# Kernel optimization log

Hardware: AMD Instinct MI355X
Metric: run time of the kernel (lower is better)

## Reference

```python
import jax, jax.numpy as jnp
import numpy as np
from jax import lax

B, S, N, DIM = 4, 512, 16, 8
D_MODEL, D_STATE = 1024, 64
INPUT_SIZE = N * DIM
LN_EPS = 1e-5


def setup_inputs() -> dict:
    key = jax.random.key(0)
    ks = jax.random.split(key, 8)
    s = 0.02
    x = jax.random.normal(ks[0], (B, S, N, DIM), dtype=jnp.float32)
    W_emb = jax.random.normal(ks[1], (INPUT_SIZE, D_MODEL), dtype=jnp.float32) * s
    b_emb = jnp.zeros((D_MODEL,), jnp.float32)
    W_xp = jax.random.normal(ks[2], (D_MODEL, 2 * D_STATE + 1), dtype=jnp.float32) * s
    b_xp = jnp.zeros((2 * D_STATE + 1,), jnp.float32)
    # A init: -exp(arange(1, d_state+1) * 0.1), matching the torch module
    A = -jnp.exp(jnp.arange(1, D_STATE + 1, dtype=jnp.float32) * 0.1)
    Dp = jnp.ones((D_MODEL,), jnp.float32)
    gamma = jnp.ones((D_MODEL,), jnp.float32)
    beta = jnp.zeros((D_MODEL,), jnp.float32)
    W_out = jax.random.normal(ks[3], (D_MODEL, INPUT_SIZE), dtype=jnp.float32) * s
    b_out = jnp.zeros((INPUT_SIZE,), jnp.float32)
    return {"x": x, "W_emb": W_emb, "b_emb": b_emb, "W_xp": W_xp, "b_xp": b_xp,
            "A": A, "Dp": Dp, "gamma": gamma, "beta": beta,
            "W_out": W_out, "b_out": b_out}


def reference(x, W_emb, b_emb, W_xp, b_xp, A, Dp, gamma, beta, W_out, b_out):
    b, s, n, dim = x.shape
    d_state = A.shape[0]
    d_model = W_emb.shape[1]
    u = x.reshape(b, s, n * dim) @ W_emb + b_emb            # [B,S,dm]
    sel = u @ W_xp + b_xp                                    # [B,S,2*ds+1]
    delta = jax.nn.softplus(sel[..., 0:1]) * 0.01            # [B,S,1]
    Bs = sel[..., 1:1 + d_state]                             # [B,S,ds]
    Cs = sel[..., 1 + d_state:]                              # [B,S,ds]
    A_bar = jnp.exp(delta * A)                               # [B,S,ds]
    B_bar = delta * Bs                                       # [B,S,ds]

    def step(h, inp):
        a_t, b_t, c_t, u_t = inp                             # [B,ds],[B,ds],[B,ds],[B,dm]
        h = h * a_t[:, None, :] + b_t[:, None, :] * u_t[:, :, None]  # [B,dm,ds]
        y_t = jnp.einsum('bmd,bd->bm', h, c_t) + u_t * Dp
        return h, y_t

    h0 = jnp.zeros((b, d_model, d_state), x.dtype)
    xs = (jnp.swapaxes(A_bar, 0, 1), jnp.swapaxes(B_bar, 0, 1),
          jnp.swapaxes(Cs, 0, 1), jnp.swapaxes(u, 0, 1))
    _, ys = lax.scan(step, h0, xs)                           # ys: [S,B,dm]
    y = jnp.swapaxes(ys, 0, 1)                               # [B,S,dm]
    mu = y.mean(-1, keepdims=True)
    var = y.var(-1, keepdims=True)
    yn = (y - mu) / jnp.sqrt(var + LN_EPS) * gamma + beta
    pred = yn @ W_out + b_out                                # [B,S,N*D]
    return pred.reshape(b, s, n, dim)
```

## Files before the change

kernel.cpp:

```cpp
#include <hip/hip_runtime.h>
#include <cstddef>

constexpr int ROWS = 2048;
constexpr int NTC  = 16;
constexpr int CL   = 32;

__global__ __launch_bounds__(256)
void k0_rearrange(const float* __restrict__ Wxp,
                  float* __restrict__ wBC, float* __restrict__ wd) {
  int idx = blockIdx.x * 256 + threadIdx.x;
  if (idx >= 1024 * 129) return;
  int k = idx / 129;
  int c = idx - k * 129;
  float v = Wxp[idx];
  if (c == 0) wd[k] = v;
  else        wBC[k * 128 + (c - 1)] = v;
}

template<bool SPLIT>
__global__ __launch_bounds__(256)
void gemm_f32(const float* __restrict__ A, const float* __restrict__ Bm,
              const float* __restrict__ bias, float* __restrict__ C,
              int M, int N, int K, int kchunk) {
  __shared__ float As[32][68];
  __shared__ float Bs[32][68];
  const int t  = threadIdx.x;
  const int n0 = blockIdx.x * 64;
  const int m0 = blockIdx.y * 64;
  int k0 = 0, kend = K;
  if (SPLIT) { k0 = blockIdx.z * kchunk; kend = k0 + kchunk; }
  const int tx = t & 15, ty = t >> 4;
  const int arow = t >> 3, acol = (t & 7) << 2;
  const int brow = t >> 4, bcol = (t & 15) << 2;
  float acc[4][4] = {{0.f}};

  for (int kt = k0; kt < kend; kt += 32) {
    float4 a0 = *(const float4*)&A[(size_t)(m0 + arow)      * K + kt + acol];
    float4 a1 = *(const float4*)&A[(size_t)(m0 + arow + 32) * K + kt + acol];
    float4 b0 = *(const float4*)&Bm[(size_t)(kt + brow)      * N + n0 + bcol];
    float4 b1 = *(const float4*)&Bm[(size_t)(kt + brow + 16) * N + n0 + bcol];
    __syncthreads();
    As[acol + 0][arow] = a0.x; As[acol + 1][arow] = a0.y;
    As[acol + 2][arow] = a0.z; As[acol + 3][arow] = a0.w;
    As[acol + 0][arow + 32] = a1.x; As[acol + 1][arow + 32] = a1.y;
    As[acol + 2][arow + 32] = a1.z; As[acol + 3][arow + 32] = a1.w;
    *(float4*)&Bs[brow][bcol]      = b0;
    *(float4*)&Bs[brow + 16][bcol] = b1;
    __syncthreads();
    #pragma unroll
    for (int k = 0; k < 32; ++k) {
      float4 av = *(const float4*)&As[k][ty << 2];
      float4 bv = *(const float4*)&Bs[k][tx << 2];
      float a_[4] = {av.x, av.y, av.z, av.w};
      float b_[4] = {bv.x, bv.y, bv.z, bv.w};
      #pragma unroll
      for (int i = 0; i < 4; ++i)
        #pragma unroll
        for (int j = 0; j < 4; ++j)
          acc[i][j] = fmaf(a_[i], b_[j], acc[i][j]);
    }
  }

  float* Cp = C;
  if (SPLIT) Cp += (size_t)blockIdx.z * (size_t)M * N;
  #pragma unroll
  for (int i = 0; i < 4; ++i) {
    int row = m0 + (ty << 2) + i;
    float4 v = make_float4(acc[i][0], acc[i][1], acc[i][2], acc[i][3]);
    if (!SPLIT && bias) {
      float4 bb = *(const float4*)&bias[n0 + (tx << 2)];
      v.x += bb.x; v.y += bb.y; v.z += bb.z; v.w += bb.w;
    }
    *(float4*)&Cp[(size_t)row * N + n0 + (tx << 2)] = v;
  }
}

__global__ __launch_bounds__(256)
void k2d_gemv(const float* __restrict__ u, const float* __restrict__ wd,
              float* __restrict__ d_raw) {
  int t = threadIdx.x, lane = t & 63, wv = t >> 6;
  int row = blockIdx.x * 4 + wv;
  const float* up = u + (size_t)row * 1024;
  float acc = 0.f;
  #pragma unroll
  for (int i = 0; i < 16; ++i)
    acc = fmaf(up[lane + i * 64], wd[lane + i * 64], acc);
  #pragma unroll
  for (int o = 32; o; o >>= 1) acc += __shfl_xor(acc, o, 64);
  if (lane == 0) d_raw[row] = acc;
}

__global__ __launch_bounds__(256)
void k2e_epilogue(const float* __restrict__ part, const float* __restrict__ d_raw,
                  const float* __restrict__ bxp, const float* __restrict__ A,
                  float* __restrict__ abc) {
  int gid = blockIdx.x * 256 + threadIdx.x;
  int row = gid >> 6, d = gid & 63;
  const size_t PN = (size_t)ROWS * 128;
  float sb = 0.f, sc = 0.f;
  #pragma unroll
  for (int z = 0; z < 4; ++z) {
    sb += part[z * PN + (size_t)row * 128 + d];
    sc += part[z * PN + (size_t)row * 128 + 64 + d];
  }
  sb += bxp[1 + d];
  sc += bxp[65 + d];
  float x = d_raw[row] + bxp[0];
  float sp = (x > 15.f) ? x : log1pf(__expf(x));
  float delta = 0.01f * sp;
  float* o = abc + (size_t)row * 192;
  o[d]       = __expf(delta * A[d]);
  o[64 + d]  = delta * sb;
  o[128 + d] = sc;
}


__global__ __launch_bounds__(256)
void scan_sum(const float* __restrict__ u, const float* __restrict__ abc,
              float* __restrict__ cst, float* __restrict__ Ach) {
  __shared__ __align__(16) float sbuf[CL * 192];
  const int t = threadIdx.x, lane = t & 63, w = t >> 6;
  const int tc = blockIdx.x % 15;
  const int mg = (blockIdx.x / 15) & 3;
  const int b  = blockIdx.x / 60;
  const int r0 = b * 512 + tc * CL;

  const float4* src = (const float4*)(abc + (size_t)r0 * 192);
  #pragma unroll
  for (int i = 0; i < 6; ++i)
    ((float4*)sbuf)[t + i * 256] = src[t + i * 256];
  __syncthreads();

  const int m = (mg * 4 + w) * 64 + lane;
  const float* ub = u + (size_t)r0 * 1024 + m;
  const bool doAp = (mg == 0 && w == 0);

  float2 h[32];
  float2 ap[32];
  #pragma unroll
  for (int j = 0; j < 32; ++j) { h[j] = make_float2(0.f, 0.f); ap[j] = make_float2(1.f, 1.f); }

  float u0 = ub[0];
  float u1 = ub[1024];
  for (int s = 0; s < CL; ++s) {
    int sn = (s < CL - 3) ? s + 2 : CL - 1;
    float u2 = ub[(size_t)sn * 1024];
    const float* L = sbuf + s * 192;
    #pragma unroll
    for (int jj = 0; jj < 16; ++jj) {
      float4 a4 = *(const float4*)&L[4 * jj];
      float4 b4 = *(const float4*)&L[64 + 4 * jj];
      h[2 * jj].x     = fmaf(h[2 * jj].x,     a4.x, b4.x * u0);
      h[2 * jj].y     = fmaf(h[2 * jj].y,     a4.y, b4.y * u0);
      h[2 * jj + 1].x = fmaf(h[2 * jj + 1].x, a4.z, b4.z * u0);
      h[2 * jj + 1].y = fmaf(h[2 * jj + 1].y, a4.w, b4.w * u0);
    }
    if (doAp) {
      #pragma unroll
      for (int jj = 0; jj < 16; ++jj) {
        float4 a4 = *(const float4*)&L[4 * jj];
        ap[2 * jj].x     *= a4.x;
        ap[2 * jj].y     *= a4.y;
        ap[2 * jj + 1].x *= a4.z;
        ap[2 * jj + 1].y *= a4.w;
      }
    }
    u0 = u1; u1 = u2;
  }

  size_t cbase = (((size_t)b * 15 + tc) * 64) * 1024 + m;
  #pragma unroll
  for (int j = 0; j < 32; ++j) {
    cst[cbase + (size_t)(2 * j)     * 1024] = h[j].x;
    cst[cbase + (size_t)(2 * j + 1) * 1024] = h[j].y;
  }
  if (doAp && lane == 0) {
    float2* ad = (float2*)&Ach[((size_t)b * 15 + tc) * 64];
    #pragma unroll
    for (int j = 0; j < 32; ++j) ad[j] = ap[j];
  }
}

__global__ __launch_bounds__(256)
void scan_comb(float* __restrict__ cst, const float* __restrict__ Ach) {
  int g = blockIdx.x * 256 + threadIdx.x;
  int b = g >> 16;
  int rem = g & 65535;
  int d = rem >> 10;
  int m = rem & 1023;
  float h = 0.f;
  for (int t2 = 0; t2 < 15; ++t2) {
    size_t idx = (((size_t)(b * 15 + t2)) * 64 + d) * 1024 + m;
    h = fmaf(Ach[(b * 15 + t2) * 64 + d], h, cst[idx]);
    cst[idx] = h;
  }
}

__global__ __launch_bounds__(256)
void scan_out(const float* __restrict__ u, const float* __restrict__ abc,
              const float* __restrict__ cst, const float* __restrict__ Dp,
              float* __restrict__ y) {
  __shared__ __align__(16) float sbuf[CL * 192];
  const int t = threadIdx.x, lane = t & 63, w = t >> 6;
  const int tc = blockIdx.x & 15;
  const int mg = (blockIdx.x >> 4) & 3;
  const int b  = blockIdx.x >> 6;
  const int r0 = b * 512 + tc * CL;

  const float4* src = (const float4*)(abc + (size_t)r0 * 192);
  #pragma unroll
  for (int i = 0; i < 6; ++i)
    ((float4*)sbuf)[t + i * 256] = src[t + i * 256];
  __syncthreads();

  const int m = (mg * 4 + w) * 64 + lane;
  const float* ub = u + (size_t)r0 * 1024 + m;
  float*       yb = y + (size_t)r0 * 1024 + m;
  const float dp = Dp[m];

  float2 h[32];
  if (tc == 0) {
    #pragma unroll
    for (int j = 0; j < 32; ++j) h[j] = make_float2(0.f, 0.f);
  } else {
    size_t cbase = (((size_t)b * 15 + (tc - 1)) * 64) * 1024 + m;
    #pragma unroll
    for (int j = 0; j < 32; ++j) {
      h[j].x = cst[cbase + (size_t)(2 * j)     * 1024];
      h[j].y = cst[cbase + (size_t)(2 * j + 1) * 1024];
    }
  }

  float u0 = ub[0];
  float u1 = ub[1024];
  for (int s = 0; s < CL; ++s) {
    int sn = (s < CL - 3) ? s + 2 : CL - 1;
    float u2 = ub[(size_t)sn * 1024];
    const float* L = sbuf + s * 192;
    float y0 = 0.f, y1 = 0.f, y2 = 0.f, y3 = 0.f;
    #pragma unroll
    for (int jj = 0; jj < 16; ++jj) {
      float4 a4 = *(const float4*)&L[4 * jj];
      float4 b4 = *(const float4*)&L[64 + 4 * jj];
      float4 c4 = *(const float4*)&L[128 + 4 * jj];
      h[2 * jj].x     = fmaf(h[2 * jj].x,     a4.x, b4.x * u0);
      h[2 * jj].y     = fmaf(h[2 * jj].y,     a4.y, b4.y * u0);
      h[2 * jj + 1].x = fmaf(h[2 * jj + 1].x, a4.z, b4.z * u0);
      h[2 * jj + 1].y = fmaf(h[2 * jj + 1].y, a4.w, b4.w * u0);
      y0 = fmaf(c4.x, h[2 * jj].x,     y0);
      y1 = fmaf(c4.y, h[2 * jj].y,     y1);
      y2 = fmaf(c4.z, h[2 * jj + 1].x, y2);
      y3 = fmaf(c4.w, h[2 * jj + 1].y, y3);
    }
    yb[(size_t)s * 1024] = (y0 + y1) + (y2 + y3) + u0 * dp;
    u0 = u1; u1 = u2;
  }
}

__global__ __launch_bounds__(256)
void k4a_ln(const float* __restrict__ y, const float* __restrict__ gamma,
            const float* __restrict__ beta, float* __restrict__ yn) {
  __shared__ float red[8];
  int t = threadIdx.x, lane = t & 63, wv = t >> 6;
  int row = blockIdx.x;
  float4 v = *(const float4*)&y[(size_t)row * 1024 + t * 4];
  float s1 = v.x + v.y + v.z + v.w;
  float s2 = v.x * v.x + v.y * v.y + v.z * v.z + v.w * v.w;
  #pragma unroll
  for (int o = 32; o; o >>= 1) {
    s1 += __shfl_xor(s1, o, 64);
    s2 += __shfl_xor(s2, o, 64);
  }
  if (lane == 0) { red[wv] = s1; red[4 + wv] = s2; }
  __syncthreads();
  float S1 = red[0] + red[1] + red[2] + red[3];
  float S2 = red[4] + red[5] + red[6] + red[7];
  float mean = S1 * (1.f / 1024.f);
  float var  = S2 * (1.f / 1024.f) - mean * mean;
  float rstd = rsqrtf(var + 1e-5f);
  float4 g  = *(const float4*)&gamma[t * 4];
  float4 be = *(const float4*)&beta[t * 4];
  float4 o;
  o.x = (v.x - mean) * rstd * g.x + be.x;
  o.y = (v.y - mean) * rstd * g.y + be.y;
  o.z = (v.z - mean) * rstd * g.z + be.z;
  o.w = (v.w - mean) * rstd * g.w + be.w;
  *(float4*)&yn[(size_t)row * 1024 + t * 4] = o;
}

__global__ __launch_bounds__(256)
void k4c_out(const float* __restrict__ part, const float* __restrict__ bout,
             float* __restrict__ out) {
  int g4 = blockIdx.x * 256 + threadIdx.x;
  size_t idx = (size_t)g4 * 4;
  const size_t PN = (size_t)ROWS * 128;
  float4 s = *(const float4*)&part[idx];
  #pragma unroll
  for (int z = 1; z < 4; ++z) {
    float4 p = *(const float4*)&part[z * PN + idx];
    s.x += p.x; s.y += p.y; s.z += p.z; s.w += p.w;
  }
  float4 bb = *(const float4*)&bout[idx & 127];
  s.x += bb.x; s.y += bb.y; s.z += bb.z; s.w += bb.w;
  *(float4*)&out[idx] = s;
}

extern "C" void kernel_launch(void* const* d_in, const int* in_sizes, int n_in,
                              void* d_out, int out_size, void* d_ws, size_t ws_size,
                              hipStream_t stream) {
  const float* x     = (const float*)d_in[0];
  const float* W_emb = (const float*)d_in[1];
  const float* b_emb = (const float*)d_in[2];
  const float* W_xp  = (const float*)d_in[3];
  const float* b_xp  = (const float*)d_in[4];
  const float* A     = (const float*)d_in[5];
  const float* Dp    = (const float*)d_in[6];
  const float* gamma = (const float*)d_in[7];
  const float* beta  = (const float*)d_in[8];
  const float* W_out = (const float*)d_in[9];
  const float* b_out = (const float*)d_in[10];
  float* out = (float*)d_out;
  float* ws  = (float*)d_ws;

  float* u    = ws;
  float* abc  = ws + 2097152;
  float* y    = ws + 2490368;
  float* wBC  = ws + 4587520;
  float* wd   = ws + 4718592;
  float* dr   = ws + 4719616;
  float* part = ws + 4721664;
  float* cst  = ws + 5770240;
  float* Ach  = ws + 9702400;
  float* yn   = u;

  k0_rearrange<<<(1024 * 129 + 255) / 256, 256, 0, stream>>>(W_xp, wBC, wd);
  gemm_f32<false><<<dim3(16, 32, 1), 256, 0, stream>>>(x, W_emb, b_emb, u,
                                                       2048, 1024, 128, 0);
  k2d_gemv<<<512, 256, 0, stream>>>(u, wd, dr);
  gemm_f32<true><<<dim3(2, 32, 4), 256, 0, stream>>>(u, wBC, nullptr, part,
                                                     2048, 128, 1024, 256);
  k2e_epilogue<<<512, 256, 0, stream>>>(part, dr, b_xp, A, abc);
  scan_sum<<<240, 256, 0, stream>>>(u, abc, cst, Ach);
  scan_comb<<<1024, 256, 0, stream>>>(cst, Ach);
  scan_out<<<256, 256, 0, stream>>>(u, abc, cst, Dp, y);
  k4a_ln<<<2048, 256, 0, stream>>>(y, gamma, beta, yn);
  gemm_f32<true><<<dim3(2, 32, 4), 256, 0, stream>>>(yn, W_out, nullptr, part,
                                                     2048, 128, 1024, 256);
  k4c_out<<<256, 256, 0, stream>>>(part, b_out, out);
}
```

Baseline: 180.1 us.

## Switch GEMMs to bf16 MFMA with transposed weights and fused delta projection

Replaces the fp32 FMA tiled GEMMs with a bf16 MFMA 16x16x32 kernel that uses a swizzled LDS layout and pre-transposed bf16 weights. A prep kernel converts x and all weights to bf16 each call. The delta GEMV is folded into the selection GEMM as an extra padded column, and split-K goes from 4 to 8 slices. This aims to cut GEMM compute time, at the cost of bf16 precision loss in all projections and extra conversion traffic.

Measured after the change: 156.6 us. 13.1% less time.

```diff
diff --git a/kernel.cpp b/kernel.cpp
--- a/kernel.cpp
+++ b/kernel.cpp
@@ -1,119 +1,140 @@
 #include <hip/hip_runtime.h>
 #include <cstddef>
 
+typedef __attribute__((ext_vector_type(8))) short short8;
+typedef __attribute__((ext_vector_type(4))) float f32x4;
+
 constexpr int ROWS = 2048;
-constexpr int NTC  = 16;
 constexpr int CL   = 32;
 
-__global__ __launch_bounds__(256)
-void k0_rearrange(const float* __restrict__ Wxp,
-                  float* __restrict__ wBC, float* __restrict__ wd) {
+__device__ inline ushort tobf(float f) {
+  union { float f; unsigned u; } v; v.f = f;
+  return (ushort)((v.u + 0x7FFFu + ((v.u >> 16) & 1u)) >> 16);
+}
+
+__global__ __launch_bounds__(256)
+void prep(const float* __restrict__ Wemb, const float* __restrict__ Wxp,
+          const float* __restrict__ Wout, const float* __restrict__ x,
+          ushort* __restrict__ WembT, ushort* __restrict__ wBCdT,
+          ushort* __restrict__ WoutT, ushort* __restrict__ xbf) {
   int idx = blockIdx.x * 256 + threadIdx.x;
-  if (idx >= 1024 * 129) return;
-  int k = idx / 129;
-  int c = idx - k * 129;
-  float v = Wxp[idx];
-  if (c == 0) wd[k] = v;
-  else        wBC[k * 128 + (c - 1)] = v;
+  if (idx < 131072) {
+    int n = idx >> 7, k = idx & 127;
+    WembT[idx] = tobf(Wemb[k * 1024 + n]);
+  } else if (idx < 327680) {
+    int j = idx - 131072;
+    int n = j >> 10, k = j & 1023;
+    float v = (n < 128) ? Wxp[k * 129 + 1 + n] : (n == 128 ? Wxp[k * 129] : 0.f);
+    wBCdT[j] = tobf(v);
+  } else if (idx < 458752) {
+    int j = idx - 327680;
+    int n = j >> 10, k = j & 1023;
+    WoutT[j] = tobf(Wout[k * 128 + n]);
+  } else if (idx < 720896) {
+    int j = idx - 458752;
+    xbf[j] = tobf(x[j]);
+  }
 }
 
 template<bool SPLIT>
 __global__ __launch_bounds__(256)
-void gemm_f32(const float* __restrict__ A, const float* __restrict__ Bm,
-              const float* __restrict__ bias, float* __restrict__ C,
-              int M, int N, int K, int kchunk) {
-  __shared__ float As[32][68];
-  __shared__ float Bs[32][68];
+void gemm_bt_bf16(const ushort* __restrict__ A, const ushort* __restrict__ BT,
+                  const float* __restrict__ bias, float* __restrict__ C,
+                  ushort* __restrict__ Cbf, int M, int N, int K) {
+  __shared__ __align__(16) ushort sA[8192];
+  __shared__ __align__(16) ushort sB[8192];
   const int t  = threadIdx.x;
   const int n0 = blockIdx.x * 64;
   const int m0 = blockIdx.y * 64;
-  int k0 = 0, kend = K;
-  if (SPLIT) { k0 = blockIdx.z * kchunk; kend = k0 + kchunk; }
-  const int tx = t & 15, ty = t >> 4;
-  const int arow = t >> 3, acol = (t & 7) << 2;
-  const int brow = t >> 4, bcol = (t & 15) << 2;
-  float acc[4][4] = {{0.f}};
-
-  for (int kt = k0; kt < kend; kt += 32) {
-    float4 a0 = *(const float4*)&A[(size_t)(m0 + arow)      * K + kt + acol];
-    float4 a1 = *(const float4*)&A[(size_t)(m0 + arow + 32) * K + kt + acol];
-    float4 b0 = *(const float4*)&Bm[(size_t)(kt + brow)      * N + n0 + bcol];
-    float4 b1 = *(const float4*)&Bm[(size_t)(kt + brow + 16) * N + n0 + bcol];
-    __syncthreads();
-    As[acol + 0][arow] = a0.x; As[acol + 1][arow] = a0.y;
-    As[acol + 2][arow] = a0.z; As[acol + 3][arow] = a0.w;
-    As[acol + 0][arow + 32] = a1.x; As[acol + 1][arow + 32] = a1.y;
-    As[acol + 2][arow + 32] = a1.z; As[acol + 3][arow + 32] = a1.w;
-    *(float4*)&Bs[brow][bcol]      = b0;
-    *(float4*)&Bs[brow + 16][bcol] = b1;
-    __syncthreads();
-    #pragma unroll
-    for (int k = 0; k < 32; ++k) {
-      float4 av = *(const float4*)&As[k][ty << 2];
-      float4 bv = *(const float4*)&Bs[k][tx << 2];
-      float a_[4] = {av.x, av.y, av.z, av.w};
-      float b_[4] = {bv.x, bv.y, bv.z, bv.w};
-      #pragma unroll
-      for (int i = 0; i < 4; ++i)
-        #pragma unroll
-        for (int j = 0; j < 4; ++j)
-          acc[i][j] = fmaf(a_[i], b_[j], acc[i][j]);
-    }
-  }
-
+  const int kc = blockIdx.z << 7;
+
+  #pragma unroll
+  for (int i = 0; i < 4; ++i) {
+    int c = t + (i << 8);
+    int row = c >> 4, kk = (c & 15) << 3;
+    float4 va = *(const float4*)(A  + (size_t)(m0 + row) * K + kc + kk);
+    float4 vb = *(const float4*)(BT + (size_t)(n0 + row) * K + kc + kk);
+    int byteoff = ((row << 8) + (kk << 1)) ^ ((row & 7) << 4);
+    *(float4*)((char*)sA + byteoff) = va;
+    *(float4*)((char*)sB + byteoff) = vb;
+  }
+  __syncthreads();
+
+  const int lane = t & 63, w = t >> 6;
+  const int wr = w << 4;
+  const int colsel = lane & 15;
+  const int kg = lane >> 4;
+
+  short8 a[4];
+  {
+    int arow = wr + colsel;
+    int lin = (arow << 8) + (kg << 4);
+    int swz = (arow & 7) << 4;
+    #pragma unroll
+    for (int ks = 0; ks < 4; ++ks)
+      a[ks] = *(const short8*)((const char*)sA + ((lin + (ks << 6)) ^ swz));
+  }
+
+  f32x4 acc[4];
+  #pragma unroll
+  for (int nf = 0; nf < 4; ++nf) acc[nf] = (f32x4)(0.f);
+
+  #pragma unroll
+  for (int nf = 0; nf < 4; ++nf) {
+    int brow = (nf << 4) + colsel;
+    int lin = (brow << 8) + (kg << 4);
+    int swz = (brow & 7) << 4;
+    #pragma unroll
+    for (int ks = 0; ks < 4; ++ks) {
+      short8 b = *(const short8*)((const char*)sB + ((lin + (ks << 6)) ^ swz));
+      acc[nf] = __builtin_amdgcn_mfma_f32_16x16x32_bf16(a[ks], b, acc[nf], 0, 0, 0);
+    }
+  }
+
+  const int r4 = kg << 2;
   float* Cp = C;
   if (SPLIT) Cp += (size_t)blockIdx.z * (size_t)M * N;
   #pragma unroll
-  for (int i = 0; i < 4; ++i) {
-    int row = m0 + (ty << 2) + i;
-    float4 v = make_float4(acc[i][0], acc[i][1], acc[i][2], acc[i][3]);
-    if (!SPLIT && bias) {
-      float4 bb = *(const float4*)&bias[n0 + (tx << 2)];
-      v.x += bb.x; v.y += bb.y; v.z += bb.z; v.w += bb.w;
-    }
-    *(float4*)&Cp[(size_t)row * N + n0 + (tx << 2)] = v;
-  }
-}
-
-__global__ __launch_bounds__(256)
-void k2d_gemv(const float* __restrict__ u, const float* __restrict__ wd,
-              float* __restrict__ d_raw) {
-  int t = threadIdx.x, lane = t & 63, wv = t >> 6;
-  int row = blockIdx.x * 4 + wv;
-  const float* up = u + (size_t)row * 1024;
-  float acc = 0.f;
-  #pragma unroll
-  for (int i = 0; i < 16; ++i)
-    acc = fmaf(up[lane + i * 64], wd[lane + i * 64], acc);
-  #pragma unroll
-  for (int o = 32; o; o >>= 1) acc += __shfl_xor(acc, o, 64);
-  if (lane == 0) d_raw[row] = acc;
-}
-
-__global__ __launch_bounds__(256)
-void k2e_epilogue(const float* __restrict__ part, const float* __restrict__ d_raw,
-                  const float* __restrict__ bxp, const float* __restrict__ A,
-                  float* __restrict__ abc) {
+  for (int nf = 0; nf < 4; ++nf) {
+    int gn = n0 + (nf << 4) + colsel;
+    #pragma unroll
+    for (int reg = 0; reg < 4; ++reg) {
+      int gm = m0 + wr + r4 + reg;
+      if (SPLIT) {
+        Cp[(size_t)gm * N + gn] = acc[nf][reg];
+      } else {
+        float v = acc[nf][reg] + bias[gn];
+        C[(size_t)gm * N + gn] = v;
+        Cbf[(size_t)gm * N + gn] = tobf(v);
+      }
+    }
+  }
+}
+
+__global__ __launch_bounds__(256)
+void k2e_epilogue(const float* __restrict__ part, const float* __restrict__ bxp,
+                  const float* __restrict__ A, float* __restrict__ abc) {
   int gid = blockIdx.x * 256 + threadIdx.x;
   int row = gid >> 6, d = gid & 63;
-  const size_t PN = (size_t)ROWS * 128;
-  float sb = 0.f, sc = 0.f;
-  #pragma unroll
-  for (int z = 0; z < 4; ++z) {
-    sb += part[z * PN + (size_t)row * 128 + d];
-    sc += part[z * PN + (size_t)row * 128 + 64 + d];
+  const size_t PN = (size_t)ROWS * 192;
+  float sb = 0.f, sc = 0.f, dr = 0.f;
+  #pragma unroll
+  for (int z = 0; z < 8; ++z) {
+    const float* p = part + z * PN + (size_t)row * 192;
+    sb += p[d];
+    sc += p[64 + d];
+    dr += p[128];
   }
   sb += bxp[1 + d];
   sc += bxp[65 + d];
-  float x = d_raw[row] + bxp[0];
-  float sp = (x > 15.f) ? x : log1pf(__expf(x));
+  float xv = dr + bxp[0];
+  float sp = (xv > 15.f) ? xv : log1pf(__expf(xv));
   float delta = 0.01f * sp;
   float* o = abc + (size_t)row * 192;
   o[d]       = __expf(delta * A[d]);
   o[64 + d]  = delta * sb;
   o[128 + d] = sc;
 }
-
 
 __global__ __launch_bounds__(256)
 void scan_sum(const float* __restrict__ u, const float* __restrict__ abc,
@@ -259,7 +280,7 @@
 
 __global__ __launch_bounds__(256)
 void k4a_ln(const float* __restrict__ y, const float* __restrict__ gamma,
-            const float* __restrict__ beta, float* __restrict__ yn) {
+            const float* __restrict__ beta, ushort* __restrict__ ynbf) {
   __shared__ float red[8];
   int t = threadIdx.x, lane = t & 63, wv = t >> 6;
   int row = blockIdx.x;
@@ -280,12 +301,12 @@
   float rstd = rsqrtf(var + 1e-5f);
   float4 g  = *(const float4*)&gamma[t * 4];
   float4 be = *(const float4*)&beta[t * 4];
-  float4 o;
-  o.x = (v.x - mean) * rstd * g.x + be.x;
-  o.y = (v.y - mean) * rstd * g.y + be.y;
-  o.z = (v.z - mean) * rstd * g.z + be.z;
-  o.w = (v.w - mean) * rstd * g.w + be.w;
-  *(float4*)&yn[(size_t)row * 1024 + t * 4] = o;
+  ushort4 o;
+  o.x = tobf((v.x - mean) * rstd * g.x + be.x);
+  o.y = tobf((v.y - mean) * rstd * g.y + be.y);
+  o.z = tobf((v.z - mean) * rstd * g.z + be.z);
+  o.w = tobf((v.w - mean) * rstd * g.w + be.w);
+  *(ushort4*)&ynbf[(size_t)row * 1024 + t * 4] = o;
 }
 
 __global__ __launch_bounds__(256)
@@ -296,7 +317,7 @@
   const size_t PN = (size_t)ROWS * 128;
   float4 s = *(const float4*)&part[idx];
   #pragma unroll
-  for (int z = 1; z < 4; ++z) {
+  for (int z = 1; z < 8; ++z) {
     float4 p = *(const float4*)&part[z * PN + idx];
     s.x += p.x; s.y += p.y; s.z += p.z; s.w += p.w;
   }
@@ -323,28 +344,29 @@
   float* ws  = (float*)d_ws;
 
   float* u    = ws;
-  float* abc  = ws + 2097152;
-  float* y    = ws + 2490368;
-  float* wBC  = ws + 4587520;
-  float* wd   = ws + 4718592;
-  float* dr   = ws + 4719616;
-  float* part = ws + 4721664;
-  float* cst  = ws + 5770240;
-  float* Ach  = ws + 9702400;
-  float* yn   = u;
-
-  k0_rearrange<<<(1024 * 129 + 255) / 256, 256, 0, stream>>>(W_xp, wBC, wd);
-  gemm_f32<false><<<dim3(16, 32, 1), 256, 0, stream>>>(x, W_emb, b_emb, u,
-                                                       2048, 1024, 128, 0);
-  k2d_gemv<<<512, 256, 0, stream>>>(u, wd, dr);
-  gemm_f32<true><<<dim3(2, 32, 4), 256, 0, stream>>>(u, wBC, nullptr, part,
-                                                     2048, 128, 1024, 256);
-  k2e_epilogue<<<512, 256, 0, stream>>>(part, dr, b_xp, A, abc);
+  float* y    = u + 2097152;
+  float* abc  = y + 2097152;
+  float* part = abc + 393216;
+  float* cst  = part + 3145728;
+  float* Ach  = cst + 3932160;
+  ushort* ubf   = (ushort*)(Ach + 4096);
+  ushort* ynbf  = ubf + 2097152;
+  ushort* xbf   = ynbf + 2097152;
+  ushort* WembT = xbf + 262144;
+  ushort* wBCdT = WembT + 131072;
+  ushort* WoutT = wBCdT + 196608;
+
+  prep<<<2816, 256, 0, stream>>>(W_emb, W_xp, W_out, x, WembT, wBCdT, WoutT, xbf);
+  gemm_bt_bf16<false><<<dim3(16, 32, 1), 256, 0, stream>>>(
+      xbf, WembT, b_emb, u, ubf, 2048, 1024, 128);
+  gemm_bt_bf16<true><<<dim3(3, 32, 8), 256, 0, stream>>>(
+      ubf, wBCdT, nullptr, part, nullptr, 2048, 192, 1024);
+  k2e_epilogue<<<512, 256, 0, stream>>>(part, b_xp, A, abc);
   scan_sum<<<240, 256, 0, stream>>>(u, abc, cst, Ach);
   scan_comb<<<1024, 256, 0, stream>>>(cst, Ach);
   scan_out<<<256, 256, 0, stream>>>(u, abc, cst, Dp, y);
-  k4a_ln<<<2048, 256, 0, stream>>>(y, gamma, beta, yn);
-  gemm_f32<true><<<dim3(2, 32, 4), 256, 0, stream>>>(yn, W_out, nullptr, part,
-                                                     2048, 128, 1024, 256);
+  k4a_ln<<<2048, 256, 0, stream>>>(y, gamma, beta, ynbf);
+  gemm_bt_bf16<true><<<dim3(2, 32, 8), 256, 0, stream>>>(
+      ynbf, WoutT, nullptr, part, nullptr, 2048, 128, 1024);
   k4c_out<<<256, 256, 0, stream>>>(part, b_out, out);
 }
```
